# Performance work log

Measured on AMD Instinct MI355X. Metric: run time of the kernel, lower is better.

The kernel has to match this reference:

```python
import jax, jax.numpy as jnp
import numpy as np

DIM_Q = 1024
DIM_KV = 768
N_HEADS = 4


def setup_inputs() -> dict:
    key = jax.random.key(0)
    ks = jax.random.split(key, 7)
    b, lq, lkv = 4, 2048, 2048
    q = jax.random.normal(ks[0], (b, lq, DIM_Q), dtype=jnp.float32)
    kv = jax.random.normal(ks[1], (b, lkv, DIM_KV), dtype=jnp.float32)
    s_q = 1.0 / np.sqrt(DIM_Q)
    s_kv = 1.0 / np.sqrt(DIM_KV)
    Wq = jax.random.normal(ks[2], (DIM_Q, DIM_Q), dtype=jnp.float32) * s_q
    Wk = jax.random.normal(ks[3], (DIM_Q, DIM_KV), dtype=jnp.float32) * s_kv
    Wv = jax.random.normal(ks[4], (DIM_Q, DIM_KV), dtype=jnp.float32) * s_kv
    Wo = jax.random.normal(ks[5], (DIM_Q, DIM_Q), dtype=jnp.float32) * s_q
    bo = jax.random.normal(ks[6], (DIM_Q,), dtype=jnp.float32) * 0.01
    return {"q": q, "kv": kv, "Wq": Wq, "Wk": Wk, "Wv": Wv, "Wo": Wo, "bo": bo}


def _split_heads(x):
    # [b, l, d] -> [b, h, l, d/h]
    b, l, d = x.shape
    return x.reshape(b, l, N_HEADS, d // N_HEADS).transpose(0, 2, 1, 3)


def reference(q, kv, Wq, Wk, Wv, Wo, bo):
    qp = q @ Wq.T               # [b, lq, dim_q]
    kp = kv @ Wk.T              # [b, lkv, dim_q]
    vp = kv @ Wv.T              # [b, lkv, dim_q]
    qh, kh, vh = _split_heads(qp), _split_heads(kp), _split_heads(vp)
    scale = (DIM_Q // N_HEADS) ** (-0.5)
    scores = jnp.einsum('bhqd,bhkd->bhqk', qh, kh) * scale
    attn = jax.nn.softmax(scores, axis=-1)
    ctx = jnp.einsum('bhqk,bhkd->bhqd', attn, vh)  # [b, h, lq, hd]
    b, h, lq, hd = ctx.shape
    ctx = ctx.transpose(0, 2, 1, 3).reshape(b, lq, h * hd)
    return ctx @ Wo.T + bo
```

## Files before the change

### kernel.cpp

```cpp
#include <hip/hip_runtime.h>

#define DIMQ 1024
#define NH 4
#define HD 256
#define BSZ 4
#define LQ 2048
#define LKV 2048
#define KVN 2048

typedef __attribute__((ext_vector_type(8))) short bf16x8;
typedef __attribute__((ext_vector_type(4))) float f32x4;

__device__ inline unsigned short f32_to_bf16(float f) {
  union { float f; unsigned u; } v; v.f = f;
  unsigned u = v.u;
  return (unsigned short)((u + 0x7fffu + ((u >> 16) & 1u)) >> 16);
}

__device__ inline uint4 ld8cvt(const float* p, float scale) {
  const float4 a = *(const float4*)p;
  const float4 b = *(const float4*)(p + 4);
  union { unsigned short s[8]; uint4 v; } r;
  r.s[0] = f32_to_bf16(a.x * scale); r.s[1] = f32_to_bf16(a.y * scale);
  r.s[2] = f32_to_bf16(a.z * scale); r.s[3] = f32_to_bf16(a.w * scale);
  r.s[4] = f32_to_bf16(b.x * scale); r.s[5] = f32_to_bf16(b.y * scale);
  r.s[6] = f32_to_bf16(b.z * scale); r.s[7] = f32_to_bf16(b.w * scale);
  return r.v;
}

__device__ __forceinline__ void gl2lds16(const void* gptr, void* lptr) {
  __builtin_amdgcn_global_load_lds(
      (const __attribute__((address_space(1))) void*)gptr,
      (__attribute__((address_space(3))) void*)lptr, 16, 0, 0);
}

__global__ __launch_bounds__(256)
void cvt5(const float* s0, const float* s1, const float* s2, const float* s3,
          const float* s4, unsigned short* d0, unsigned short* d1,
          unsigned short* d2, unsigned short* d3, unsigned short* d4,
          long n0, long n1, long n2, long n3, long n4,
          float c0, float c1, float c2, float c3, float c4) {
  const float* s; unsigned short* d; long n; float c;
  switch (blockIdx.y) {
    case 0: s = s0; d = d0; n = n0; c = c0; break;
    case 1: s = s1; d = d1; n = n1; c = c1; break;
    case 2: s = s2; d = d2; n = n2; c = c2; break;
    case 3: s = s3; d = d3; n = n3; c = c3; break;
    default: s = s4; d = d4; n = n4; c = c4; break;
  }
  long i = ((long)blockIdx.x * 256 + threadIdx.x) * 8;
  if (i < n) *(uint4*)(d + i) = ld8cvt(s + i, c);
}

__global__ __launch_bounds__(256)
void transpose_k(const unsigned short* __restrict__ vp,
                 unsigned short* __restrict__ vpT,
                 int src_stride, int src_off) {
  __shared__ unsigned short T[64][72];
  const int l0g = blockIdx.x * 64;
  const int b = l0g / LKV, l0 = l0g % LKV;
  const int n0 = blockIdx.y * 64;
  const int tid = threadIdx.x;
  const int r = tid >> 3, c = tid & 7;
#pragma unroll
  for (int p = 0; p < 2; ++p) {
    int row = p * 32 + r;
    *(uint4*)&T[row][c * 8] =
        *(const uint4*)(vp + (size_t)(l0g + row) * src_stride + src_off + n0 + c * 8);
  }
  __syncthreads();
#pragma unroll
  for (int p = 0; p < 2; ++p) {
    int n = p * 32 + r;
    union { unsigned short s[8]; uint4 v; } t;
#pragma unroll
    for (int j = 0; j < 8; ++j) t.s[j] = T[c * 8 + j][n];
    *(uint4*)(vpT + ((size_t)b * DIMQ + n0 + n) * LKV + l0 + c * 8) = t.v;
  }
}

template<typename TOUT, bool HAS_BIAS>
__global__ __launch_bounds__(256)
void gemm_bt(const unsigned short* __restrict__ A,
             const unsigned short* __restrict__ Bm,
             const float* __restrict__ bias,
             TOUT* __restrict__ C,
             int M, int N, int K) {
  __shared__ alignas(16) unsigned short As[128 * 64];
  __shared__ alignas(16) unsigned short Bs[128 * 64];
  const int tid = threadIdx.x;
  const int lane = tid & 63;
  const int wave = tid >> 6;
  const int wr = (wave >> 1) * 64, wc = (wave & 1) * 64;
  const int l15 = lane & 15, quad = lane >> 4;
  const int srow = lane >> 3, scol = lane & 7;
  const int m0 = blockIdx.x * 128;
  const int n0 = blockIdx.y * 128;

  f32x4 acc[4][4] = {};
  for (int k0 = 0; k0 < K; k0 += 64) {
    __syncthreads();
#pragma unroll
    for (int i = 0; i < 4; ++i) {
      int c = wave * 4 + i;
      gl2lds16(A + (size_t)(m0 + c * 8 + srow) * K + k0 + scol * 8, As + c * 512);
      gl2lds16(Bm + (size_t)(n0 + c * 8 + srow) * K + k0 + scol * 8, Bs + c * 512);
    }
    __syncthreads();
#pragma unroll
    for (int kh = 0; kh < 2; ++kh) {
      bf16x8 af[4], bfr[4];
#pragma unroll
      for (int i = 0; i < 4; ++i)
        af[i] = *(const bf16x8*)(As + (wr + i * 16 + l15) * 64 + kh * 32 + quad * 8);
#pragma unroll
      for (int j = 0; j < 4; ++j)
        bfr[j] = *(const bf16x8*)(Bs + (wc + j * 16 + l15) * 64 + kh * 32 + quad * 8);
#pragma unroll
      for (int i = 0; i < 4; ++i)
#pragma unroll
        for (int j = 0; j < 4; ++j)
          acc[i][j] = __builtin_amdgcn_mfma_f32_16x16x32_bf16(af[i], bfr[j], acc[i][j], 0, 0, 0);
    }
  }

#pragma unroll
  for (int j = 0; j < 4; ++j) {
    int n = n0 + wc + j * 16 + l15;
    float bv = 0.f;
    if (HAS_BIAS) bv = bias[n];
#pragma unroll
    for (int i = 0; i < 4; ++i) {
      int mb = m0 + wr + i * 16 + quad * 4;
#pragma unroll
      for (int r = 0; r < 4; ++r) {
        float v = acc[i][j][r] + bv;
        if constexpr (sizeof(TOUT) == 2)
          C[(size_t)(mb + r) * N + n] = f32_to_bf16(v);
        else
          C[(size_t)(mb + r) * N + n] = v;
      }
    }
  }
}

__global__ __launch_bounds__(256, 2)
void attn(const unsigned short* __restrict__ qp,
          const unsigned short* __restrict__ kpv,
          const unsigned short* __restrict__ vpT,
          unsigned short* __restrict__ ctx) {
  __shared__ alignas(16) unsigned short Ks[8 * 64 * 32];
  __shared__ alignas(16) unsigned short Vt[2 * 256 * 32];
  __shared__ alignas(16) unsigned short Ps[64 * 72];
  __shared__ float Ls[64][2];
  const int tid = threadIdx.x, lane = tid & 63, wave = tid >> 6;
  const int l15 = lane & 15, quad = lane >> 4;
  const int lr = lane >> 2, lc = lane & 3;
  const int qh = wave >> 1;
  const int kvh = wave & 1;
  const int b = blockIdx.z, h = blockIdx.y;
  const int q0 = blockIdx.x * 64;
  const size_t base = (size_t)b * LQ * DIMQ + h * HD;

  bf16x8 qf[2][8];
#pragma unroll
  for (int im = 0; im < 2; ++im) {
    const unsigned short* qrow =
        qp + base + (size_t)(q0 + qh * 32 + im * 16 + l15) * DIMQ;
#pragma unroll
    for (int s = 0; s < 8; ++s)
      qf[im][s] = *(const bf16x8*)(qrow + s * 32 + quad * 8);
  }

  f32x4 oacc[2][8] = {};
  float lrow[2][4] = {};

  const unsigned short* kb = kpv + (size_t)b * LKV * KVN + h * HD;
  const unsigned short* vtb = vpT + ((size_t)b * DIMQ + h * HD) * LKV;

  for (int kv0 = 0; kv0 < LKV; kv0 += 64) {
    __syncthreads();
#pragma unroll
    for (int i = 0; i < 8; ++i) {
      int c = i * 4 + wave, s = c & 7, g = c >> 3;
      gl2lds16(kb + (size_t)(kv0 + g * 16 + lr) * KVN + s * 32 + lc * 8,
               Ks + s * 2048 + g * 512);
    }
#pragma unroll
    for (int i = 0; i < 8; ++i) {
      int c = i * 4 + wave, u = c >> 4, g = c & 15;
      gl2lds16(vtb + (size_t)(g * 16 + lr) * LKV + kv0 + u * 32 + lc * 8,
               Vt + u * 8192 + g * 512);
    }
    __syncthreads();

    f32x4 sacc[2][2] = {};
#pragma unroll
    for (int s = 0; s < 8; ++s) {
      bf16x8 kf0 = *(const bf16x8*)(Ks + s * 2048 + (kvh * 32 + l15) * 32 + quad * 8);
      bf16x8 kf1 = *(const bf16x8*)(Ks + s * 2048 + (kvh * 32 + 16 + l15) * 32 + quad * 8);
      sacc[0][0] = __builtin_amdgcn_mfma_f32_16x16x32_bf16(qf[0][s], kf0, sacc[0][0], 0, 0, 0);
      sacc[0][1] = __builtin_amdgcn_mfma_f32_16x16x32_bf16(qf[0][s], kf1, sacc[0][1], 0, 0, 0);
      sacc[1][0] = __builtin_amdgcn_mfma_f32_16x16x32_bf16(qf[1][s], kf0, sacc[1][0], 0, 0, 0);
      sacc[1][1] = __builtin_amdgcn_mfma_f32_16x16x32_bf16(qf[1][s], kf1, sacc[1][1], 0, 0, 0);
    }

#pragma unroll
    for (int im = 0; im < 2; ++im)
#pragma unroll
      for (int i = 0; i < 4; ++i) {
        int row = qh * 32 + im * 16 + quad * 4 + i;
        float p0 = __expf(sacc[im][0][i]);
        float p1 = __expf(sacc[im][1][i]);
        Ps[row * 72 + kvh * 32 + l15] = f32_to_bf16(p0);
        Ps[row * 72 + kvh * 32 + 16 + l15] = f32_to_bf16(p1);
        lrow[im][i] += p0 + p1;
      }
    __syncthreads();

#pragma unroll
    for (int u = 0; u < 2; ++u) {
      bf16x8 pf0 = *(const bf16x8*)(Ps + (qh * 32 + l15) * 72 + u * 32 + quad * 8);
      bf16x8 pf1 = *(const bf16x8*)(Ps + (qh * 32 + 16 + l15) * 72 + u * 32 + quad * 8);
#pragma unroll
      for (int jn = 0; jn < 8; ++jn) {
        bf16x8 vf = *(const bf16x8*)(Vt + u * 8192 + (kvh * 128 + jn * 16 + l15) * 32 + quad * 8);
        oacc[0][jn] = __builtin_amdgcn_mfma_f32_16x16x32_bf16(pf0, vf, oacc[0][jn], 0, 0, 0);
        oacc[1][jn] = __builtin_amdgcn_mfma_f32_16x16x32_bf16(pf1, vf, oacc[1][jn], 0, 0, 0);
      }
    }
  }

#pragma unroll
  for (int im = 0; im < 2; ++im)
#pragma unroll
    for (int i = 0; i < 4; ++i) {
      float l = lrow[im][i];
      l += __shfl_xor(l, 1);
      l += __shfl_xor(l, 2);
      l += __shfl_xor(l, 4);
      l += __shfl_xor(l, 8);
      if (l15 == 0) Ls[qh * 32 + im * 16 + quad * 4 + i][kvh] = l;
    }
  __syncthreads();

  unsigned short* cb = ctx + base;
#pragma unroll
  for (int im = 0; im < 2; ++im)
#pragma unroll
    for (int r = 0; r < 4; ++r) {
      int row = qh * 32 + im * 16 + quad * 4 + r;
      float inv = 1.0f / (Ls[row][0] + Ls[row][1]);
#pragma unroll
      for (int jn = 0; jn < 8; ++jn) {
        int col = kvh * 128 + jn * 16 + l15;
        cb[(size_t)(q0 + row) * DIMQ + col] = f32_to_bf16(oacc[im][jn][r] * inv);
      }
    }
}

extern "C" void kernel_launch(void* const* d_in, const int* in_sizes, int n_in,
                              void* d_out, int out_size, void* d_ws, size_t ws_size,
                              hipStream_t stream) {
  const float* q  = (const float*)d_in[0];
  const float* kv = (const float*)d_in[1];
  const float* Wq = (const float*)d_in[2];
  const float* Wk = (const float*)d_in[3];
  const float* Wv = (const float*)d_in[4];
  const float* Wo = (const float*)d_in[5];
  const float* bo = (const float*)d_in[6];
  float* out = (float*)d_out;

  const long NQ = (long)BSZ * LQ * DIMQ;
  const long NKV = (long)BSZ * LKV * 768;
  const long NWQ = (long)DIMQ * DIMQ;
  const long NWK = (long)DIMQ * 768;

  unsigned short* q_bf = (unsigned short*)d_out;
  unsigned short* kpv  = (unsigned short*)d_out;
  unsigned short* kv_bf = (unsigned short*)d_ws;
  unsigned short* ctx   = kv_bf;
  unsigned short* Wq_bf = kv_bf + NQ;
  unsigned short* Wk_bf = Wq_bf + NWQ;
  unsigned short* Wv_bf = Wk_bf + NWK;
  unsigned short* Wo_bf = Wv_bf + NWK;
  unsigned short* qp    = Wo_bf + NWQ;
  unsigned short* vpT   = qp + NQ;

  dim3 blk(256);
  const int M = BSZ * LQ;

  cvt5<<<dim3(3072, 5), blk, 0, stream>>>(kv, Wq, Wk, Wv, Wo,
                                          kv_bf, Wq_bf, Wk_bf, Wv_bf, Wo_bf,
                                          NKV, NWQ, NWK, NWK, NWQ,
                                          1.0f, 0.0625f, 1.0f, 1.0f, 1.0f);
  cvt5<<<dim3(4096, 1), blk, 0, stream>>>(q, nullptr, nullptr, nullptr, nullptr,
                                          q_bf, nullptr, nullptr, nullptr, nullptr,
                                          NQ, 0, 0, 0, 0,
                                          1.0f, 0.f, 0.f, 0.f, 0.f);
  gemm_bt<unsigned short, false><<<dim3(M/128, DIMQ/128), blk, 0, stream>>>(q_bf, Wq_bf, nullptr, qp, M, DIMQ, 1024);
  gemm_bt<unsigned short, false><<<dim3(M/128, KVN/128), blk, 0, stream>>>(kv_bf, Wk_bf, nullptr, kpv, M, KVN, 768);
  transpose_k<<<dim3(M/64, DIMQ/64), blk, 0, stream>>>(kpv, vpT, KVN, 1024);
  attn<<<dim3(LQ/64, NH, BSZ), blk, 0, stream>>>(qp, kpv, vpT, ctx);
  gemm_bt<float, true><<<dim3(M/128, DIMQ/128), blk, 0, stream>>>(ctx, Wo_bf, bo, out, M, DIMQ, 1024);
}
```

Before: 318.2 us.

## Swizzle LDS tiles and prefetch next K tile during PV phase

Replaces the padded LDS layouts in the transpose and attention kernels with XOR-swizzled row-major layouts, so bank conflicts are avoided without padding. It also restructures the attention loop. The first K tile is loaded before the loop, V is loaded while QK^T is computed, and the next K tile is prefetched during the PV MFMA phase. This overlaps global-to-LDS traffic with compute, at the cost of more index arithmetic and a changed barrier placement.

```diff
diff --git a/kernel.cpp b/kernel.cpp
--- a/kernel.cpp
+++ b/kernel.cpp
@@ -56,7 +56,7 @@
 void transpose_k(const unsigned short* __restrict__ vp,
                  unsigned short* __restrict__ vpT,
                  int src_stride, int src_off) {
-  __shared__ unsigned short T[64][72];
+  __shared__ unsigned short T[64][64];
   const int l0g = blockIdx.x * 64;
   const int b = l0g / LKV, l0 = l0g % LKV;
   const int n0 = blockIdx.y * 64;
@@ -65,7 +65,7 @@
 #pragma unroll
   for (int p = 0; p < 2; ++p) {
     int row = p * 32 + r;
-    *(uint4*)&T[row][c * 8] =
+    *(uint4*)&T[row][(c ^ ((row >> 3) & 7)) * 8] =
         *(const uint4*)(vp + (size_t)(l0g + row) * src_stride + src_off + n0 + c * 8);
   }
   __syncthreads();
@@ -74,7 +74,10 @@
     int n = p * 32 + r;
     union { unsigned short s[8]; uint4 v; } t;
 #pragma unroll
-    for (int j = 0; j < 8; ++j) t.s[j] = T[c * 8 + j][n];
+    for (int j = 0; j < 8; ++j) {
+      int row = c * 8 + j;
+      t.s[j] = T[row][(((n >> 3) ^ ((row >> 3) & 7)) << 3) | (n & 7)];
+    }
     *(uint4*)(vpT + ((size_t)b * DIMQ + n0 + n) * LKV + l0 + c * 8) = t.v;
   }
 }
@@ -149,13 +152,12 @@
           const unsigned short* __restrict__ kpv,
           const unsigned short* __restrict__ vpT,
           unsigned short* __restrict__ ctx) {
-  __shared__ alignas(16) unsigned short Ks[8 * 64 * 32];
-  __shared__ alignas(16) unsigned short Vt[2 * 256 * 32];
-  __shared__ alignas(16) unsigned short Ps[64 * 72];
+  __shared__ alignas(16) unsigned short Ks[64 * 256];
+  __shared__ alignas(16) unsigned short Vt[256 * 64];
+  __shared__ alignas(16) unsigned short Ps[64 * 64];
   __shared__ float Ls[64][2];
   const int tid = threadIdx.x, lane = tid & 63, wave = tid >> 6;
   const int l15 = lane & 15, quad = lane >> 4;
-  const int lr = lane >> 2, lc = lane & 3;
   const int qh = wave >> 1;
   const int kvh = wave & 1;
   const int b = blockIdx.z, h = blockIdx.y;
@@ -178,33 +180,41 @@
   const unsigned short* kb = kpv + (size_t)b * LKV * KVN + h * HD;
   const unsigned short* vtb = vpT + ((size_t)b * DIMQ + h * HD) * LKV;
 
+  const int krow_l = lane >> 5;
+  const int kcol_l = lane & 31;
+  const int vrow_l = lane >> 3;
+  const int vcol_l = lane & 7;
+
+#pragma unroll
+  for (int i = 0; i < 8; ++i) {
+    int c = i * 4 + wave;
+    int row = 2 * c + krow_l;
+    gl2lds16(kb + (size_t)row * KVN + ((kcol_l ^ (row & 7)) << 3), Ks + c * 512);
+  }
+  __syncthreads();
+
   for (int kv0 = 0; kv0 < LKV; kv0 += 64) {
-    __syncthreads();
 #pragma unroll
     for (int i = 0; i < 8; ++i) {
-      int c = i * 4 + wave, s = c & 7, g = c >> 3;
-      gl2lds16(kb + (size_t)(kv0 + g * 16 + lr) * KVN + s * 32 + lc * 8,
-               Ks + s * 2048 + g * 512);
-    }
-#pragma unroll
-    for (int i = 0; i < 8; ++i) {
-      int c = i * 4 + wave, u = c >> 4, g = c & 15;
-      gl2lds16(vtb + (size_t)(g * 16 + lr) * LKV + kv0 + u * 32 + lc * 8,
-               Vt + u * 8192 + g * 512);
-    }
-    __syncthreads();
+      int c = i * 4 + wave;
+      int row = 8 * c + vrow_l;
+      gl2lds16(vtb + (size_t)row * LKV + kv0 + ((vcol_l ^ (row & 7)) << 3),
+               Vt + c * 512);
+    }
 
     f32x4 sacc[2][2] = {};
+    const int r0 = kvh * 32 + l15, r1 = r0 + 16;
 #pragma unroll
     for (int s = 0; s < 8; ++s) {
-      bf16x8 kf0 = *(const bf16x8*)(Ks + s * 2048 + (kvh * 32 + l15) * 32 + quad * 8);
-      bf16x8 kf1 = *(const bf16x8*)(Ks + s * 2048 + (kvh * 32 + 16 + l15) * 32 + quad * 8);
+      bf16x8 kf0 = *(const bf16x8*)(Ks + r0 * 256 + (((s * 4 + quad) ^ (r0 & 7)) << 3));
+      bf16x8 kf1 = *(const bf16x8*)(Ks + r1 * 256 + (((s * 4 + quad) ^ (r1 & 7)) << 3));
       sacc[0][0] = __builtin_amdgcn_mfma_f32_16x16x32_bf16(qf[0][s], kf0, sacc[0][0], 0, 0, 0);
       sacc[0][1] = __builtin_amdgcn_mfma_f32_16x16x32_bf16(qf[0][s], kf1, sacc[0][1], 0, 0, 0);
       sacc[1][0] = __builtin_amdgcn_mfma_f32_16x16x32_bf16(qf[1][s], kf0, sacc[1][0], 0, 0, 0);
       sacc[1][1] = __builtin_amdgcn_mfma_f32_16x16x32_bf16(qf[1][s], kf1, sacc[1][1], 0, 0, 0);
     }
 
+    const int c0 = kvh * 32 + l15, c1 = c0 + 16;
 #pragma unroll
     for (int im = 0; im < 2; ++im)
 #pragma unroll
@@ -212,23 +222,36 @@
         int row = qh * 32 + im * 16 + quad * 4 + i;
         float p0 = __expf(sacc[im][0][i]);
         float p1 = __expf(sacc[im][1][i]);
-        Ps[row * 72 + kvh * 32 + l15] = f32_to_bf16(p0);
-        Ps[row * 72 + kvh * 32 + 16 + l15] = f32_to_bf16(p1);
+        Ps[row * 64 + ((((c0 >> 3) ^ (row & 7)) << 3) | (c0 & 7))] = f32_to_bf16(p0);
+        Ps[row * 64 + ((((c1 >> 3) ^ (row & 7)) << 3) | (c1 & 7))] = f32_to_bf16(p1);
         lrow[im][i] += p0 + p1;
       }
     __syncthreads();
 
+    if (kv0 + 64 < LKV) {
+#pragma unroll
+      for (int i = 0; i < 8; ++i) {
+        int c = i * 4 + wave;
+        int row = 2 * c + krow_l;
+        gl2lds16(kb + (size_t)(kv0 + 64 + row) * KVN + ((kcol_l ^ (row & 7)) << 3),
+                 Ks + c * 512);
+      }
+    }
+
+    const int pr0 = qh * 32 + l15, pr1 = pr0 + 16;
 #pragma unroll
     for (int u = 0; u < 2; ++u) {
-      bf16x8 pf0 = *(const bf16x8*)(Ps + (qh * 32 + l15) * 72 + u * 32 + quad * 8);
-      bf16x8 pf1 = *(const bf16x8*)(Ps + (qh * 32 + 16 + l15) * 72 + u * 32 + quad * 8);
+      bf16x8 pf0 = *(const bf16x8*)(Ps + pr0 * 64 + (((u * 4 + quad) ^ (pr0 & 7)) << 3));
+      bf16x8 pf1 = *(const bf16x8*)(Ps + pr1 * 64 + (((u * 4 + quad) ^ (pr1 & 7)) << 3));
 #pragma unroll
       for (int jn = 0; jn < 8; ++jn) {
-        bf16x8 vf = *(const bf16x8*)(Vt + u * 8192 + (kvh * 128 + jn * 16 + l15) * 32 + quad * 8);
+        int vr = kvh * 128 + jn * 16 + l15;
+        bf16x8 vf = *(const bf16x8*)(Vt + vr * 64 + (((u * 4 + quad) ^ (vr & 7)) << 3));
         oacc[0][jn] = __builtin_amdgcn_mfma_f32_16x16x32_bf16(pf0, vf, oacc[0][jn], 0, 0, 0);
         oacc[1][jn] = __builtin_amdgcn_mfma_f32_16x16x32_bf16(pf1, vf, oacc[1][jn], 0, 0, 0);
       }
     }
+    __syncthreads();
   }
 
 #pragma unroll
```

After: 308.4 us. -3.1%, faster.
